# Kernel tuning notes

Hardware: AMD Instinct MI355X
Metric: run time of the kernel (lower is better)

Reference implementation:

```python
import jax, jax.numpy as jnp
import numpy as np

B, T, U, V = 8, 512, 128, 128  # batch, frames, label len (U+1 pred steps), vocab incl. blank
BLANK = 0


def setup_inputs() -> dict:
    key = jax.random.key(0)
    k1, k2, k3, k4 = jax.random.split(key, 4)
    logits = jax.random.normal(k1, (B, T, U + 1, V), dtype=jnp.float32)
    y = jax.random.randint(k2, (B, U), 1, V).astype(jnp.int32)  # labels, never blank
    logit_lens = jax.random.randint(k3, (B,), T // 2, T + 1).astype(jnp.int32)
    y_lens = jax.random.randint(k4, (B,), U // 2, U + 1).astype(jnp.int32)
    batch_offset = jnp.cumsum(logit_lens * (y_lens + 1)).astype(jnp.int32)
    return {
        "logits": logits,
        "y": y,
        "logit_lens": logit_lens,
        "y_lens": y_lens,
        "batch_offset": batch_offset,
        "max_f_len": T,
    }


def _combine(e1, e2):
    # log-domain affine recurrence x[u] = logaddexp(x[u-1] + c[u], a[u])
    c1, a1 = e1
    c2, a2 = e2
    return (c1 + c2, jnp.logaddexp(a1 + c2, a2))


def rnnt_loss(logits, y, logit_lens, y_lens, blank_idx):
    Bb, Tt, U1, Vv = logits.shape
    Uu = U1 - 1
    lp = jax.nn.log_softmax(logits, axis=-1)            # [B,T,U+1,V]
    blank = lp[..., blank_idx]                          # [B,T,U+1]
    idx = jnp.broadcast_to(y[:, None, :, None], (Bb, Tt, Uu, 1)).astype(jnp.int32)
    emit = jnp.take_along_axis(lp[:, :, :Uu, :], idx, axis=3)[..., 0]  # [B,T,U]

    # alpha[0,u] = sum_{v<u} emit(0,v)
    row0 = jnp.concatenate(
        [jnp.zeros((Bb, 1), lp.dtype), jnp.cumsum(emit[:, 0, :], axis=1)], axis=1
    )  # [B,U+1]
    neg = jnp.full((Bb, 1), -jnp.inf, lp.dtype)

    def step(prev_row, x):
        bl_prev, em_t = x                               # [B,U+1], [B,U]
        a = prev_row + bl_prev                          # come-from-below (blank at t-1)
        c = jnp.concatenate([neg, em_t], axis=1)        # come-from-left (emit at t)
        _, row = jax.lax.associative_scan(_combine, (c, a), axis=1)
        return row, row

    xs = (jnp.swapaxes(blank[:, : Tt - 1, :], 0, 1), jnp.swapaxes(emit[:, 1:, :], 0, 1))
    _, rows = jax.lax.scan(step, row0, xs)              # [T-1,B,U+1]
    alphas = jnp.swapaxes(jnp.concatenate([row0[None], rows], axis=0), 0, 1)  # [B,T,U+1]

    bi = jnp.arange(Bb)
    ti = logit_lens - 1
    ui = y_lens
    ll = alphas[bi, ti, ui] + blank[bi, ti, ui]
    return -ll                                          # per-utterance negative log-lik


def reference(logits, y, logit_lens, y_lens, batch_offset, max_f_len):
    # batch_offset / max_f_len are packing metadata, unused when packed_input=False
    return rnnt_loss(logits, y, logit_lens, y_lens, BLANK).mean()
```

## Files before the change

### kernel.cpp

```cpp
#include <hip/hip_runtime.h>

#define Bb 8
#define Tt 512
#define Uu 128
#define U1 129
#define Vv 128

#define OUT_OFF 0
#define CTROW 132
#define CTROWS 321
#define CTASZ ((size_t)CTROWS * CTROW)
#define CT_BSZ (3 * CTASZ)
#define CT_OFF ((size_t)Bb * Tt * U1 * 2)
#define CTCOL_OFF (CT_OFF + (size_t)Bb * CT_BSZ)
#define RES_OFF (CTCOL_OFF + (size_t)Bb * CTROWS * 4)

#define K_LN2    0.6931471805599453f
#define K_INVLN2 1.4426950408889634f
#define SENT (-1.0e30f)

__device__ __forceinline__ float fexp2(float x) {
    float r; asm("v_exp_f32 %0, %1" : "=v"(r) : "v"(x)); return r;
}
__device__ __forceinline__ float flog2(float x) {
    float r; asm("v_log_f32 %0, %1" : "=v"(r) : "v"(x)); return r;
}

__global__ __launch_bounds__(256) void lse_kernel(
    const float* __restrict__ logits, const int* __restrict__ y,
    const int* __restrict__ logit_lens, const int* __restrict__ y_lens,
    float* __restrict__ ws)
{
    const int b = blockIdx.y;
    const int t = blockIdx.x;
    if (t >= logit_lens[b]) return;
    const int Ue = y_lens[b];

    float2* outv = (float2*)(ws + OUT_OFF);
    const int wid  = threadIdx.x >> 6;
    const int lane = threadIdx.x & 63;
    const int g    = lane >> 4;
    const int gl   = lane & 15;
    const unsigned rowbase = ((unsigned)b * Tt + t) * U1;
    const int yb = b * Uu;

    for (int u0 = wid * 8; u0 <= Ue; u0 += 32) {
        const int ua = u0 + g;
        const int ub = u0 + 4 + g;
        const int uca = ua > Ue ? Ue : ua;
        const int ucb = ub > Ue ? Ue : ub;
        const float* pa = logits + (size_t)(rowbase + uca) * Vv;
        const float* pb = logits + (size_t)(rowbase + ucb) * Vv;
        float4 a1 = *(const float4*)(pa + gl * 4);
        float4 a2 = *(const float4*)(pa + 64 + gl * 4);
        float4 b1 = *(const float4*)(pb + gl * 4);
        float4 b2 = *(const float4*)(pb + 64 + gl * 4);

        float sa = (fexp2(a1.x * K_INVLN2) + fexp2(a1.y * K_INVLN2))
                 + (fexp2(a1.z * K_INVLN2) + fexp2(a1.w * K_INVLN2))
                 + (fexp2(a2.x * K_INVLN2) + fexp2(a2.y * K_INVLN2))
                 + (fexp2(a2.z * K_INVLN2) + fexp2(a2.w * K_INVLN2));
        float sb = (fexp2(b1.x * K_INVLN2) + fexp2(b1.y * K_INVLN2))
                 + (fexp2(b1.z * K_INVLN2) + fexp2(b1.w * K_INVLN2))
                 + (fexp2(b2.x * K_INVLN2) + fexp2(b2.y * K_INVLN2))
                 + (fexp2(b2.z * K_INVLN2) + fexp2(b2.w * K_INVLN2));
        #pragma unroll
        for (int off = 8; off; off >>= 1) {
            sa += __shfl_xor(sa, off);
            sb += __shfl_xor(sb, off);
        }
        float lseA = flog2(sa);
        float lseB = flog2(sb);

        float emA = SENT, emB = SENT;
        if (uca < Uu) {
            int yv = y[yb + uca];
            int c = yv & 3;
            float4 cv = (yv & 64) ? a2 : a1;
            float cand = (c == 0) ? cv.x : (c == 1) ? cv.y : (c == 2) ? cv.z : cv.w;
            float ev = __shfl(cand, (lane & 48) | ((yv & 63) >> 2));
            emA = ev * K_INVLN2 - lseA;
        }
        if (ucb < Uu) {
            int yv = y[yb + ucb];
            int c = yv & 3;
            float4 cv = (yv & 64) ? b2 : b1;
            float cand = (c == 0) ? cv.x : (c == 1) ? cv.y : (c == 2) ? cv.z : cv.w;
            float ev = __shfl(cand, (lane & 48) | ((yv & 63) >> 2));
            emB = ev * K_INVLN2 - lseB;
        }
        if (gl == 0) {
            if (ua <= Ue) outv[rowbase + ua] = make_float2(a1.x * K_INVLN2 - lseA, emA);
            if (ub <= Ue) outv[rowbase + ub] = make_float2(b1.x * K_INVLN2 - lseB, emB);
        }
    }
}

__device__ __forceinline__ float lae2(float x, float y) {
    float dd = x - y;
    float nad = __builtin_bit_cast(float, __builtin_bit_cast(int, dd) | 0x80000000);
    return fmaxf(x, y) + flog2(1.0f + fexp2(nad));
}
__device__ __forceinline__ float lae3(float x, float y, float z) {
    float m = fmaxf(fmaxf(x, y), z);
    return m + flog2(fexp2(x - m) + fexp2(y - m) + fexp2(z - m));
}

__global__ __launch_bounds__(256) void cond_kernel(
    const int* __restrict__ logit_lens, const int* __restrict__ y_lens,
    float* __restrict__ ws)
{
    const int b = blockIdx.x / 320;
    const int m = blockIdx.x - b * 320 + 1;
    if (m > ((logit_lens[b] - 1 + y_lens[b]) >> 1)) return;
    const int r1 = 2 * m - 2, r2 = 2 * m - 1;
    const float2* outv = (const float2*)(ws + OUT_OFF);

    __shared__ float2 D1[U1], D2[U1];
    for (int q = threadIdx.x; q < 2 * U1; q += 256) {
        const int which = q >= U1;
        const int j = q - which * U1;
        const int t = (which ? r2 : r1) - j;
        float2 val = make_float2(SENT, SENT);
        if (t >= 0 && t < Tt) val = outv[((size_t)b * Tt + t) * U1 + j];
        (which ? D2 : D1)[j] = val;
    }
    __syncthreads();

    const int u = threadIdx.x;
    if (u <= 128) {
        float2 d1  = D1[u], d2 = D2[u];
        float2 d1m = (u >= 1) ? D1[u - 1] : make_float2(SENT, SENT);
        float d2my  = (u >= 1) ? D2[u - 1].y : SENT;
        float d1m2y = (u >= 2) ? D1[u - 2].y : SENT;
        float A = d1.x + d2.x;
        float B = lae2(d1m.y + d2.x, d1m.x + d2my);
        float C = d1m2y + d2my;
        float* CTAb = ws + CT_OFF + (size_t)b * CT_BSZ;
        CTAb[(size_t)m * CTROW + u]             = A;
        CTAb[CTASZ + (size_t)m * CTROW + u]     = B;
        CTAb[2 * CTASZ + (size_t)m * CTROW + u] = C;
        if (u == 128)
            ((float4*)(ws + CTCOL_OFF))[(size_t)b * CTROWS + m] = make_float4(A, B, C, 0.0f);
    }
}

template<int MODE>
__device__ __forceinline__ float rot1(float x, int lane) {
    if constexpr (MODE == 2) {
        float s = __shfl_up(x, 1);
        float w = __shfl(x, 63);
        return (lane == 0) ? w : s;
    } else {
        constexpr int CTRL = (MODE == 0) ? 0x13C : 0x134;
        int i = __builtin_bit_cast(int, x);
        i = __builtin_amdgcn_update_dpp(i, i, CTRL, 0xF, 0xF, true);
        return __builtin_bit_cast(float, i);
    }
}

template<int MODE, bool H128>
__device__ __forceinline__ void dp_body(int b, int lane, int Tb, int Ub,
                                        float* __restrict__ ws)
{
    const float2* outv = (const float2*)(ws + OUT_OFF);
    const float* CTAb = ws + CT_OFF + (size_t)b * CT_BSZ;
    const float* CTBb = CTAb + CTASZ;
    const float* CTCb = CTBb + CTASZ;
    const float4* COLb = (const float4*)(ws + CTCOL_OFF) + (size_t)b * CTROWS;
    int zv; asm volatile("v_mov_b32 %0, 0" : "=v"(zv));

    float px = (lane == 0) ? 0.0f : SENT;
    float py = SENT, p2 = SENT;
    const int dend = Tb - 1 + Ub;
    const int np   = dend >> 1;
    const int odd  = dend & 1;

    float2 F1 = make_float2(0,0), F2 = make_float2(0,0), G = make_float2(0,0);
    if (odd) {
        const int r = dend - 1;
        int j1 = 2 * lane, j2 = 2 * lane + 1;
        int t1 = r - j1; t1 = t1 > Tt - 1 ? Tt - 1 : t1;
        int t2 = r - j2; t2 = t2 > Tt - 1 ? Tt - 1 : t2;
        F1 = outv[((size_t)b * Tt + t1) * U1 + j1];
        F2 = outv[((size_t)b * Tt + t2) * U1 + j2];
        if constexpr (H128) G = outv[((size_t)b * Tt + (r - 128)) * U1 + 128];
    }
    float pbf = outv[((size_t)b * Tt + (Tb - 1)) * U1 + Ub + zv].x;

    float2 A0,A1,A2,A3,A4,A5,A6,A7,A8,A9,A10,A11;
    float2 B0,B1,B2,B3,B4,B5,B6,B7,B8,B9,B10,B11;
    float2 C0,C1,C2,C3,C4,C5,C6,C7,C8,C9,C10,C11;
    float4 O0,O1,O2,O3,O4,O5,O6,O7,O8,O9,O10,O11;

#define LOADC(i, mm) { unsigned o = (unsigned)(mm) * CTROW + 2 * lane; \
    A##i = *(const float2*)(CTAb + o); \
    B##i = *(const float2*)(CTBb + o); \
    C##i = *(const float2*)(CTCb + o); \
    if constexpr (H128) O##i = COLb[(mm) + zv]; }

#define PIN(i) if constexpr (H128) { \
        asm volatile("" : "+v"(A##i.x), "+v"(A##i.y), "+v"(B##i.x), "+v"(B##i.y), \
                          "+v"(C##i.x), "+v"(C##i.y), "+v"(O##i.x), "+v"(O##i.y), "+v"(O##i.z)); \
    } else { \
        asm volatile("" : "+v"(A##i.x), "+v"(A##i.y), "+v"(B##i.x), "+v"(B##i.y), \
                          "+v"(C##i.x), "+v"(C##i.y)); \
    }

#define COMP2(i) { \
    float pm1 = rot1<MODE>(py, lane); \
    float pm0 = rot1<MODE>(px, lane); \
    float nx = lae3(px + A##i.x, pm1 + B##i.x, pm0 + C##i.x); \
    float ny = lae3(py + A##i.y, px + B##i.y, pm1 + C##i.y); \
    if constexpr (H128) p2 = lae3(p2 + O##i.x, pm1 + O##i.y, pm0 + O##i.z); \
    px = nx; py = ny; }

    LOADC(0,1)  LOADC(1,2)  LOADC(2,3)   LOADC(3,4)
    LOADC(4,5)  LOADC(5,6)  LOADC(6,7)   LOADC(7,8)
    LOADC(8,9)  LOADC(9,10) LOADC(10,11) LOADC(11,12)

    int m = 1;
    for (; m + 11 <= np; m += 12) {
        PIN(0)  COMP2(0)  { int dn = m + 12 > np ? np : m + 12; LOADC(0,  dn) }
        PIN(1)  COMP2(1)  { int dn = m + 13 > np ? np : m + 13; LOADC(1,  dn) }
        PIN(2)  COMP2(2)  { int dn = m + 14 > np ? np : m + 14; LOADC(2,  dn) }
        PIN(3)  COMP2(3)  { int dn = m + 15 > np ? np : m + 15; LOADC(3,  dn) }
        PIN(4)  COMP2(4)  { int dn = m + 16 > np ? np : m + 16; LOADC(4,  dn) }
        PIN(5)  COMP2(5)  { int dn = m + 17 > np ? np : m + 17; LOADC(5,  dn) }
        PIN(6)  COMP2(6)  { int dn = m + 18 > np ? np : m + 18; LOADC(6,  dn) }
        PIN(7)  COMP2(7)  { int dn = m + 19 > np ? np : m + 19; LOADC(7,  dn) }
        PIN(8)  COMP2(8)  { int dn = m + 20 > np ? np : m + 20; LOADC(8,  dn) }
        PIN(9)  COMP2(9)  { int dn = m + 21 > np ? np : m + 21; LOADC(9,  dn) }
        PIN(10) COMP2(10) { int dn = m + 22 > np ? np : m + 22; LOADC(10, dn) }
        PIN(11) COMP2(11) { int dn = m + 23 > np ? np : m + 23; LOADC(11, dn) }
    }
#define TAILC(i) if (m <= np) { PIN(i) COMP2(i) m++; }
    TAILC(0) TAILC(1) TAILC(2) TAILC(3) TAILC(4) TAILC(5)
    TAILC(6) TAILC(7) TAILC(8) TAILC(9) TAILC(10)

    if (odd) {
        float pm  = rot1<MODE>(py, lane);
        float pmE = rot1<MODE>(F2.y, lane);
        float pmE0 = (lane == 0) ? SENT : pmE;
        float nx = lae2(px + F1.x, pm + pmE0);
        float ny = lae2(py + F2.x, px + F1.y);
        if constexpr (H128) p2 = lae2(p2 + G.x, pm + pmE);
        px = nx; py = ny;
    }

    float a;
    if constexpr (H128) {
        a = __shfl(p2, 0);
    } else {
        float ax = __shfl(px, Ub >> 1);
        float ay = __shfl(py, Ub >> 1);
        a = (Ub & 1) ? ay : ax;
    }
    if (lane == 0) {
        ws[RES_OFF + b] = -(a + pbf) * K_LN2;
    }
#undef LOADC
#undef PIN
#undef COMP2
#undef TAILC
}

__global__ __launch_bounds__(64) void dp_kernel(
    const int* __restrict__ logit_lens, const int* __restrict__ y_lens,
    float* __restrict__ ws)
{
    const int b = blockIdx.x;
    const int lane = threadIdx.x;
    const int Tb = logit_lens[b];
    const int Ub = y_lens[b];
    const bool h = (Ub == 128);
    int li = lane;
    int r0 = __builtin_amdgcn_update_dpp(li, li, 0x13C , 0xF, 0xF, true);
    int r1 = __builtin_amdgcn_update_dpp(li, li, 0x134 , 0xF, 0xF, true);
    int want = (lane + 63) & 63;
    if (__all(r0 == want)) {
        if (h) dp_body<0, true>(b, lane, Tb, Ub, ws);
        else   dp_body<0, false>(b, lane, Tb, Ub, ws);
    } else if (__all(r1 == want)) {
        if (h) dp_body<1, true>(b, lane, Tb, Ub, ws);
        else   dp_body<1, false>(b, lane, Tb, Ub, ws);
    } else {
        if (h) dp_body<2, true>(b, lane, Tb, Ub, ws);
        else   dp_body<2, false>(b, lane, Tb, Ub, ws);
    }
}

__global__ void mean_kernel(const float* __restrict__ res, float* __restrict__ out)
{
    if (threadIdx.x == 0) {
        float s = 0.0f;
        #pragma unroll
        for (int i = 0; i < Bb; ++i) s += res[i];
        out[0] = s * (1.0f / Bb);
    }
}

extern "C" void kernel_launch(void* const* d_in, const int* in_sizes, int n_in,
                              void* d_out, int out_size, void* d_ws, size_t ws_size,
                              hipStream_t stream) {
    const float* logits     = (const float*)d_in[0];
    const int*   y          = (const int*)d_in[1];
    const int*   logit_lens = (const int*)d_in[2];
    const int*   y_lens     = (const int*)d_in[3];
    float* ws  = (float*)d_ws;
    float* out = (float*)d_out;

    dim3 lgrid(Tt, Bb);
    lse_kernel<<<lgrid, 256, 0, stream>>>(logits, y, logit_lens, y_lens, ws);
    cond_kernel<<<Bb * 320, 256, 0, stream>>>(logit_lens, y_lens, ws);
    dp_kernel<<<Bb, 64, 0, stream>>>(logit_lens, y_lens, ws);
    mean_kernel<<<1, 64, 0, stream>>>(ws + RES_OFF, out);
}
```

Measured before the change: 70.53 us.

## Pack per-row A/B/C coefficients into interleaved layout, deepen prefetch, use max3

cond_kernel now stages its A/B/C coefficients in shared memory and writes them out as one interleaved row of 8 floats per lane pair. The DP loop can then fetch each step's coefficients with one float4 load and one float2 load instead of three separate float2 loads from three arrays. The software prefetch depth in the serial DP loop grows from 12 to 16 rows, and lae3 uses v_max3_f32. In exchange, the workspace grows from 132 to 512 floats per row, there is an extra __syncthreads and copy loop in cond_kernel, and the deeper prefetch needs more registers.

```diff
diff --git a/kernel.cpp b/kernel.cpp
--- a/kernel.cpp
+++ b/kernel.cpp
@@ -7,12 +7,11 @@
 #define Vv 128
 
 #define OUT_OFF 0
-#define CTROW 132
 #define CTROWS 321
-#define CTASZ ((size_t)CTROWS * CTROW)
-#define CT_BSZ (3 * CTASZ)
-#define CT_OFF ((size_t)Bb * Tt * U1 * 2)
-#define CTCOL_OFF (CT_OFF + (size_t)Bb * CT_BSZ)
+#define PCKROW 512
+#define PCKBSZ ((size_t)CTROWS * PCKROW)
+#define PCK_OFF ((size_t)Bb * Tt * U1 * 2)
+#define CTCOL_OFF (PCK_OFF + (size_t)Bb * PCKBSZ)
 #define RES_OFF (CTCOL_OFF + (size_t)Bb * CTROWS * 4)
 
 #define K_LN2    0.6931471805599453f
@@ -24,6 +23,10 @@
 }
 __device__ __forceinline__ float flog2(float x) {
     float r; asm("v_log_f32 %0, %1" : "=v"(r) : "v"(x)); return r;
+}
+__device__ __forceinline__ float fmax3(float x, float y, float z) {
+    float r; asm("v_max3_f32 %0, %1, %2, %3" : "=v"(r) : "v"(x), "v"(y), "v"(z));
+    return r;
 }
 
 __global__ __launch_bounds__(256) void lse_kernel(
@@ -102,7 +105,7 @@
     return fmaxf(x, y) + flog2(1.0f + fexp2(nad));
 }
 __device__ __forceinline__ float lae3(float x, float y, float z) {
-    float m = fmaxf(fmaxf(x, y), z);
+    float m = fmax3(x, y, z);
     return m + flog2(fexp2(x - m) + fexp2(y - m) + fexp2(z - m));
 }
 
@@ -117,6 +120,7 @@
     const float2* outv = (const float2*)(ws + OUT_OFF);
 
     __shared__ float2 D1[U1], D2[U1];
+    __shared__ float pckS[PCKROW];
     for (int q = threadIdx.x; q < 2 * U1; q += 256) {
         const int which = q >= U1;
         const int j = q - which * U1;
@@ -136,13 +140,20 @@
         float A = d1.x + d2.x;
         float B = lae2(d1m.y + d2.x, d1m.x + d2my);
         float C = d1m2y + d2my;
-        float* CTAb = ws + CT_OFF + (size_t)b * CT_BSZ;
-        CTAb[(size_t)m * CTROW + u]             = A;
-        CTAb[CTASZ + (size_t)m * CTROW + u]     = B;
-        CTAb[2 * CTASZ + (size_t)m * CTROW + u] = C;
-        if (u == 128)
+        if (u < 128) {
+            int base = (u >> 1) * 8 + (u & 1);
+            pckS[base]     = A;
+            pckS[base + 2] = B;
+            pckS[base + 4] = C;
+            if ((u & 1) == 0) { pckS[base + 6] = 0.0f; pckS[base + 7] = 0.0f; }
+        } else {
             ((float4*)(ws + CTCOL_OFF))[(size_t)b * CTROWS + m] = make_float4(A, B, C, 0.0f);
-    }
+        }
+    }
+    __syncthreads();
+
+    float* pckG = ws + PCK_OFF + (size_t)b * PCKBSZ + (size_t)m * PCKROW;
+    for (int i = threadIdx.x; i < PCKROW; i += 256) pckG[i] = pckS[i];
 }
 
 template<int MODE>
@@ -164,9 +175,7 @@
                                         float* __restrict__ ws)
 {
     const float2* outv = (const float2*)(ws + OUT_OFF);
-    const float* CTAb = ws + CT_OFF + (size_t)b * CT_BSZ;
-    const float* CTBb = CTAb + CTASZ;
-    const float* CTCb = CTBb + CTASZ;
+    const float* PCKb = ws + PCK_OFF + (size_t)b * PCKBSZ;
     const float4* COLb = (const float4*)(ws + CTCOL_OFF) + (size_t)b * CTROWS;
     int zv; asm volatile("v_mov_b32 %0, 0" : "=v"(zv));
 
@@ -188,55 +197,59 @@
     }
     float pbf = outv[((size_t)b * Tt + (Tb - 1)) * U1 + Ub + zv].x;
 
-    float2 A0,A1,A2,A3,A4,A5,A6,A7,A8,A9,A10,A11;
-    float2 B0,B1,B2,B3,B4,B5,B6,B7,B8,B9,B10,B11;
-    float2 C0,C1,C2,C3,C4,C5,C6,C7,C8,C9,C10,C11;
-    float4 O0,O1,O2,O3,O4,O5,O6,O7,O8,O9,O10,O11;
-
-#define LOADC(i, mm) { unsigned o = (unsigned)(mm) * CTROW + 2 * lane; \
-    A##i = *(const float2*)(CTAb + o); \
-    B##i = *(const float2*)(CTBb + o); \
-    C##i = *(const float2*)(CTCb + o); \
+    float4 Q0,Q1,Q2,Q3,Q4,Q5,Q6,Q7,Q8,Q9,Q10,Q11,Q12,Q13,Q14,Q15;
+    float2 R0,R1,R2,R3,R4,R5,R6,R7,R8,R9,R10,R11,R12,R13,R14,R15;
+    float4 O0,O1,O2,O3,O4,O5,O6,O7,O8,O9,O10,O11,O12,O13,O14,O15;
+
+#define LOADC(i, mm) { unsigned o = (unsigned)(mm) * PCKROW + (lane << 3); \
+    Q##i = *(const float4*)(PCKb + o); \
+    R##i = *(const float2*)(PCKb + o + 4); \
     if constexpr (H128) O##i = COLb[(mm) + zv]; }
 
 #define PIN(i) if constexpr (H128) { \
-        asm volatile("" : "+v"(A##i.x), "+v"(A##i.y), "+v"(B##i.x), "+v"(B##i.y), \
-                          "+v"(C##i.x), "+v"(C##i.y), "+v"(O##i.x), "+v"(O##i.y), "+v"(O##i.z)); \
+        asm volatile("" : "+v"(Q##i.x), "+v"(Q##i.y), "+v"(Q##i.z), "+v"(Q##i.w), \
+                          "+v"(R##i.x), "+v"(R##i.y), "+v"(O##i.x), "+v"(O##i.y), "+v"(O##i.z)); \
     } else { \
-        asm volatile("" : "+v"(A##i.x), "+v"(A##i.y), "+v"(B##i.x), "+v"(B##i.y), \
-                          "+v"(C##i.x), "+v"(C##i.y)); \
+        asm volatile("" : "+v"(Q##i.x), "+v"(Q##i.y), "+v"(Q##i.z), "+v"(Q##i.w), \
+                          "+v"(R##i.x), "+v"(R##i.y)); \
     }
 
 #define COMP2(i) { \
     float pm1 = rot1<MODE>(py, lane); \
     float pm0 = rot1<MODE>(px, lane); \
-    float nx = lae3(px + A##i.x, pm1 + B##i.x, pm0 + C##i.x); \
-    float ny = lae3(py + A##i.y, px + B##i.y, pm1 + C##i.y); \
+    float nx = lae3(px + Q##i.x, pm1 + Q##i.z, pm0 + R##i.x); \
+    float ny = lae3(py + Q##i.y, px + Q##i.w, pm1 + R##i.y); \
     if constexpr (H128) p2 = lae3(p2 + O##i.x, pm1 + O##i.y, pm0 + O##i.z); \
     px = nx; py = ny; }
 
-    LOADC(0,1)  LOADC(1,2)  LOADC(2,3)   LOADC(3,4)
-    LOADC(4,5)  LOADC(5,6)  LOADC(6,7)   LOADC(7,8)
-    LOADC(8,9)  LOADC(9,10) LOADC(10,11) LOADC(11,12)
+    LOADC(0,1)   LOADC(1,2)   LOADC(2,3)   LOADC(3,4)
+    LOADC(4,5)   LOADC(5,6)   LOADC(6,7)   LOADC(7,8)
+    LOADC(8,9)   LOADC(9,10)  LOADC(10,11) LOADC(11,12)
+    LOADC(12,13) LOADC(13,14) LOADC(14,15) LOADC(15,16)
 
     int m = 1;
-    for (; m + 11 <= np; m += 12) {
-        PIN(0)  COMP2(0)  { int dn = m + 12 > np ? np : m + 12; LOADC(0,  dn) }
-        PIN(1)  COMP2(1)  { int dn = m + 13 > np ? np : m + 13; LOADC(1,  dn) }
-        PIN(2)  COMP2(2)  { int dn = m + 14 > np ? np : m + 14; LOADC(2,  dn) }
-        PIN(3)  COMP2(3)  { int dn = m + 15 > np ? np : m + 15; LOADC(3,  dn) }
-        PIN(4)  COMP2(4)  { int dn = m + 16 > np ? np : m + 16; LOADC(4,  dn) }
-        PIN(5)  COMP2(5)  { int dn = m + 17 > np ? np : m + 17; LOADC(5,  dn) }
-        PIN(6)  COMP2(6)  { int dn = m + 18 > np ? np : m + 18; LOADC(6,  dn) }
-        PIN(7)  COMP2(7)  { int dn = m + 19 > np ? np : m + 19; LOADC(7,  dn) }
-        PIN(8)  COMP2(8)  { int dn = m + 20 > np ? np : m + 20; LOADC(8,  dn) }
-        PIN(9)  COMP2(9)  { int dn = m + 21 > np ? np : m + 21; LOADC(9,  dn) }
-        PIN(10) COMP2(10) { int dn = m + 22 > np ? np : m + 22; LOADC(10, dn) }
-        PIN(11) COMP2(11) { int dn = m + 23 > np ? np : m + 23; LOADC(11, dn) }
+    for (; m + 15 <= np; m += 16) {
+        PIN(0)  COMP2(0)  { int dn = m + 16 > np ? np : m + 16; LOADC(0,  dn) }
+        PIN(1)  COMP2(1)  { int dn = m + 17 > np ? np : m + 17; LOADC(1,  dn) }
+        PIN(2)  COMP2(2)  { int dn = m + 18 > np ? np : m + 18; LOADC(2,  dn) }
+        PIN(3)  COMP2(3)  { int dn = m + 19 > np ? np : m + 19; LOADC(3,  dn) }
+        PIN(4)  COMP2(4)  { int dn = m + 20 > np ? np : m + 20; LOADC(4,  dn) }
+        PIN(5)  COMP2(5)  { int dn = m + 21 > np ? np : m + 21; LOADC(5,  dn) }
+        PIN(6)  COMP2(6)  { int dn = m + 22 > np ? np : m + 22; LOADC(6,  dn) }
+        PIN(7)  COMP2(7)  { int dn = m + 23 > np ? np : m + 23; LOADC(7,  dn) }
+        PIN(8)  COMP2(8)  { int dn = m + 24 > np ? np : m + 24; LOADC(8,  dn) }
+        PIN(9)  COMP2(9)  { int dn = m + 25 > np ? np : m + 25; LOADC(9,  dn) }
+        PIN(10) COMP2(10) { int dn = m + 26 > np ? np : m + 26; LOADC(10, dn) }
+        PIN(11) COMP2(11) { int dn = m + 27 > np ? np : m + 27; LOADC(11, dn) }
+        PIN(12) COMP2(12) { int dn = m + 28 > np ? np : m + 28; LOADC(12, dn) }
+        PIN(13) COMP2(13) { int dn = m + 29 > np ? np : m + 29; LOADC(13, dn) }
+        PIN(14) COMP2(14) { int dn = m + 30 > np ? np : m + 30; LOADC(14, dn) }
+        PIN(15) COMP2(15) { int dn = m + 31 > np ? np : m + 31; LOADC(15, dn) }
     }
 #define TAILC(i) if (m <= np) { PIN(i) COMP2(i) m++; }
-    TAILC(0) TAILC(1) TAILC(2) TAILC(3) TAILC(4) TAILC(5)
-    TAILC(6) TAILC(7) TAILC(8) TAILC(9) TAILC(10)
+    TAILC(0)  TAILC(1)  TAILC(2)  TAILC(3)  TAILC(4)
+    TAILC(5)  TAILC(6)  TAILC(7)  TAILC(8)  TAILC(9)
+    TAILC(10) TAILC(11) TAILC(12) TAILC(13) TAILC(14)
 
     if (odd) {
         float pm  = rot1<MODE>(py, lane);
```

Result: no change. 69.45 us (-1.5%).
